# Kernel optimization log

Hardware: AMD Instinct MI355X
Metric: run time of the kernel (lower is better)

The kernel has to match this reference:

```python
import jax, jax.numpy as jnp
import numpy as np
from jax import lax

DN = ('NCHW', 'OIHW', 'NCHW')

def _conv(x, w, b):
    y = lax.conv_general_dilated(x, w, (1, 1), 'SAME', dimension_numbers=DN)
    return y + b[None, :, None, None]

def setup_inputs() -> dict:
    key = jax.random.key(0)
    ks = jax.random.split(key, 12)
    B, C, H, W = 8, 32, 128, 128
    Cb, INT, K, FK = 64, 64, 3, 3
    inp = {
        'z': jax.random.normal(ks[0], (B, C, H, W), jnp.float32),
        'backbone': jax.random.normal(ks[1], (B, Cb, H, W), jnp.float32),
        'mem_stab': jax.random.normal(ks[2], (B, C, H, W), jnp.float32),
        'mem_unstab': jax.random.normal(ks[3], (B, C, H, W), jnp.float32),
        'w0': jax.random.normal(ks[4], (INT, Cb + 3 * C, K, K), jnp.float32) * 0.05,
        'b0': jnp.zeros((INT,), jnp.float32),
        'w1': jax.random.normal(ks[5], (INT, INT, K, K), jnp.float32) * 0.05,
        'b1': jnp.zeros((INT,), jnp.float32),
        'w2': jax.random.normal(ks[6], (INT, INT, K, K), jnp.float32) * 0.05,
        'b2': jnp.zeros((INT,), jnp.float32),
        'w_last': jax.random.normal(ks[7], (C * FK * FK, INT, K, K), jnp.float32) * 0.05,
        'b_last': jnp.full((C * FK * FK,), -4.0, jnp.float32),
        'fusion_kernel_size': FK,
    }
    return inp

def reference(z, backbone, mem_stab, mem_unstab, w0, b0, w1, b1, w2, b2, w_last, b_last, fusion_kernel_size):
    B, C, H, W = z.shape
    k = int(fusion_kernel_size)
    p = k * k
    # controller conv stack (LeakyReLU slope 0.01, matching nn.LeakyReLU default)
    q = jnp.concatenate([backbone, z, mem_stab, mem_unstab], axis=1)
    q = jax.nn.leaky_relu(_conv(q, w0, b0), 0.01)
    q = jax.nn.leaky_relu(_conv(q, w1, b1), 0.01)
    q = jax.nn.leaky_relu(_conv(q, w2, b2), 0.01)
    # fusion head -> [B, C, p, HW]
    head = _conv(q, w_last, b_last).reshape(B, C, p, H * W)
    # softmax over p kernel positions + one extra logit-0 slot for z itself
    eta = jax.nn.softmax(jnp.concatenate([head, jnp.zeros_like(head[:, :, :1])], axis=2), axis=2)
    # unfold(mem_stab, k, padding=k//2): patches ordered (c, kh, kw) like torch unfold
    pad = k // 2
    mpad = jnp.pad(mem_stab, ((0, 0), (0, 0), (pad, pad), (pad, pad)))
    patches = jnp.stack([mpad[:, :, i:i + H, j:j + W] for i in range(k) for j in range(k)], axis=2)
    patches = patches.reshape(B, C, p, H * W)
    z_flat = z.reshape(B, C, H * W)
    z_stab = (patches * eta[:, :, :p]).sum(axis=2) + eta[:, :, p] * z_flat
    return z_stab.reshape(B, C, H, W)
```

## Files before the change

### kernel.cpp

```cpp
#include <hip/hip_runtime.h>
#include <hip/hip_fp16.h>

typedef _Float16 half8 __attribute__((ext_vector_type(8)));
typedef _Float16 half4v __attribute__((ext_vector_type(4)));
typedef float floatx4 __attribute__((ext_vector_type(4)));

#define HW 128
#define IMG (HW * HW)
#define PH 130
#define XP 164

typedef __attribute__((address_space(3))) _Float16 lds_f16;
typedef __attribute__((address_space(1))) const _Float16 glb_f16;
__device__ __forceinline__ void gload16(const _Float16* g, _Float16* l) {
    __builtin_amdgcn_global_load_lds((glb_f16*)g, (lds_f16*)l, 16, 0, 0);
}

__global__ void pack_w_all(const float* __restrict__ w0, const float* __restrict__ w1,
                           const float* __restrict__ w2, const float* __restrict__ wl,
                           _Float16* __restrict__ p0, _Float16* __restrict__ p1,
                           _Float16* __restrict__ p2, _Float16* __restrict__ pl) {
    int idx = blockIdx.x * 256 + threadIdx.x;
    if (idx < 92160) {
        int local = idx;
        int o = local / 1440;
        int rem = local % 1440;
        int c = rem / 9;
        int t = rem % 9;
        int oh = o >> 5, n = (o >> 4) & 1, l15 = o & 15;
        int cb = c >> 5, l4 = (c >> 3) & 3, e = c & 7;
        int frag = (t * 5 + cb) * 2 + n;
        p0[(size_t)oh * 46080 + frag * 512 + (l4 * 16 + l15) * 8 + e] =
            (_Float16)w0[local];
        return;
    }
    if (idx < 165888) {
        const float* w; _Float16* p; int local;
        if (idx < 129024) { w = w1; p = p1; local = idx - 92160; }
        else              { w = w2; p = p2; local = idx - 129024; }
        int o = local / 576;
        int rem = local % 576;
        int c = rem / 9;
        int t = rem % 9;
        int oh = o >> 5, n = (o >> 4) & 1, l15 = o & 15;
        int cb = c >> 5, l4 = (c >> 3) & 3, e = c & 7;
        int frag = t * 4 + cb * 2 + n;
        p[(size_t)oh * 18432 + frag * 512 + (l4 * 16 + l15) * 8 + e] =
            (_Float16)w[local];
        return;
    }
    if (idx < 331776) {
        int local = idx - 165888;
        int of = local / 576;
        int rem = local % 576;
        int c = rem / 9;
        int t = rem % 9;
        int ct = of / 96, o = of % 96;
        int og = o / 48;
        int n = (o % 48) / 16;
        int l15 = o & 15;
        int j = c >> 3;
        int cb = j >> 2, l4 = j & 3, e = c & 7;
        int frag = t * 2 + cb;
        pl[((((size_t)(ct * 2 + og) * 18 + frag) * 3 + n) * 64
            + (l4 * 16 + l15)) * 8 + e] = (_Float16)wl[local];
    }
}

__device__ __forceinline__ void zero_halo(_Float16* P, int C, int id) {
    int nvec = C / 8;
    int b = id / (516 * nvec);
    int r = id % (516 * nvec);
    int cell = r / nvec;
    int v = r % nvec;
    int hh, ww;
    if (cell < 130)      { hh = 0;   ww = cell; }
    else if (cell < 260) { hh = 129; ww = cell - 130; }
    else if (cell < 388) { hh = cell - 260 + 1; ww = 0; }
    else                 { hh = cell - 388 + 1; ww = 129; }
    half8 z8 = {};
    *reinterpret_cast<half8*>(P + (((size_t)b * PH + hh) * PH + ww) * C + v * 8) = z8;
}

__global__ void zero_pads_pre(_Float16* __restrict__ X0, _Float16* __restrict__ Q1) {
    int id = blockIdx.x * 256 + threadIdx.x;
    if (id < 82560) zero_halo(X0, 160, id);
    else if (id < 115584) zero_halo(Q1, 64, id - 82560);
}

__global__ void zero_pads64(_Float16* __restrict__ P) {
    int id = blockIdx.x * 256 + threadIdx.x;
    if (id < 33024) zero_halo(P, 64, id);
}

__global__ __launch_bounds__(256)
void pack_in(const float* __restrict__ z, const float* __restrict__ bb,
             const float* __restrict__ ms, const float* __restrict__ mu,
             _Float16* __restrict__ X0) {
    __shared__ _Float16 lds[160 * 132];
    int b = blockIdx.x >> 7;
    int h = blockIdx.x & 127;
    int tid = threadIdx.x;

    for (int i = 0; i < 20; i++) {
        int id = i * 256 + tid;
        int c = id >> 5;
        int col = (id & 31) * 4;
        const float* src; int cs; int csz;
        if (c < 64)       { src = bb; cs = c;       csz = 64; }
        else if (c < 96)  { src = z;  cs = c - 64;  csz = 32; }
        else if (c < 128) { src = ms; cs = c - 96;  csz = 32; }
        else              { src = mu; cs = c - 128; csz = 32; }
        float4 v = *reinterpret_cast<const float4*>(
            src + ((size_t)b * csz + cs) * IMG + h * HW + col);
        half4v hv = { (_Float16)v.x, (_Float16)v.y, (_Float16)v.z, (_Float16)v.w };
        *reinterpret_cast<half4v*>(&lds[c * 132 + col]) = hv;
    }
    __syncthreads();
    _Float16* dst = X0 + (((size_t)b * PH + (h + 1)) * PH + 1) * 160;
    for (int i = 0; i < 10; i++) {
        int id = i * 256 + tid;
        int pix = id / 20;
        int c0 = (id % 20) * 8;
        half8 hv;
        #pragma unroll
        for (int e = 0; e < 8; e++) hv[e] = lds[(c0 + e) * 132 + pix];
        *reinterpret_cast<half8*>(dst + (size_t)pix * 160 + c0) = hv;
    }
}

__global__ __launch_bounds__(256, 2)
void conv3_c160(const _Float16* __restrict__ X, const _Float16* __restrict__ Wp,
                const float* __restrict__ bias, _Float16* __restrict__ Y) {
    __shared__ _Float16 xs[130 * XP];
    int b = blockIdx.x >> 7;
    int h = blockIdx.x & 127;
    int tid = threadIdx.x;
    int lane = tid & 63;
    int wave = tid >> 6;
    int ph = wave & 1;
    int oh = wave >> 1;
    int l15 = lane & 15;
    int l4  = lane >> 4;

    floatx4 acc[4][2] = {};
    half8 SA[10], SB[10];

    const _Float16* wl = Wp + (size_t)oh * 46080 + lane * 8;

#define LOADW(S, k) { \
    _Pragma("unroll") \
    for (int cb = 0; cb < 5; cb++) \
      _Pragma("unroll") \
      for (int n = 0; n < 2; n++) \
        S[cb * 2 + n] = *reinterpret_cast<const half8*>( \
            wl + (size_t)(((k) * 5 + cb) * 2 + n) * 512); }

#define STAGE160(r) { \
    const _Float16* grow = X + ((size_t)b * PH + (h + (r))) * PH * 160; \
    _Pragma("unroll") \
    for (int i = 0; i < 11; i++) { \
      int id = i * 256 + tid; \
      if (id < 2600) { \
        half8 v = *reinterpret_cast<const half8*>(grow + (size_t)id * 8); \
        *reinterpret_cast<half8*>(&xs[(id / 20) * XP + (id % 20) * 8]) = v; \
      } } }

#define COMP160(dw, S) { \
    _Pragma("unroll") \
    for (int cb = 0; cb < 5; cb++) { \
      int kofs = cb * 32 + l4 * 8; \
      half8 af[4]; \
      _Pragma("unroll") \
      for (int m = 0; m < 4; m++) { \
        int p = ph * 64 + m * 16 + l15; \
        af[m] = *reinterpret_cast<const half8*>(&xs[(p + (dw)) * XP + kofs]); \
      } \
      _Pragma("unroll") \
      for (int m = 0; m < 4; m++) \
        _Pragma("unroll") \
        for (int n = 0; n < 2; n++) \
          acc[m][n] = __builtin_amdgcn_mfma_f32_16x16x32_f16( \
              af[m], S[cb * 2 + n], acc[m][n], 0, 0, 0); } }

    LOADW(SA, 0);
    STAGE160(0);
    __syncthreads();
    LOADW(SB, 1);  COMP160(0, SA);
    LOADW(SA, 2);  COMP160(1, SB);
    LOADW(SB, 3);  COMP160(2, SA);
    __syncthreads();
    STAGE160(1);
    __syncthreads();
    LOADW(SA, 4);  COMP160(0, SB);
    LOADW(SB, 5);  COMP160(1, SA);
    LOADW(SA, 6);  COMP160(2, SB);
    __syncthreads();
    STAGE160(2);
    __syncthreads();
    LOADW(SB, 7);  COMP160(0, SA);
    LOADW(SA, 8);  COMP160(1, SB);
    COMP160(2, SA);

#undef LOADW
#undef STAGE160
#undef COMP160

    _Float16* dst = Y + (((size_t)b * PH + (h + 1)) * PH + 1) * 64;
    #pragma unroll
    for (int m = 0; m < 4; m++)
        #pragma unroll
        for (int n = 0; n < 2; n++) {
            int o = oh * 32 + n * 16 + l15;
            float bv = bias[o];
            #pragma unroll
            for (int q = 0; q < 4; q++) {
                int pix = ph * 64 + m * 16 + l4 * 4 + q;
                float v = acc[m][n][q] + bv;
                v = v > 0.f ? v : 0.01f * v;
                dst[(size_t)pix * 64 + o] = (_Float16)v;
            }
        }
}

__global__ __launch_bounds__(256, 2)
void conv3_c64(const _Float16* __restrict__ X, const _Float16* __restrict__ Wp,
               const float* __restrict__ bias, _Float16* __restrict__ Y) {
    __shared__ _Float16 xs[130 * 72];
    int b = blockIdx.x >> 7;
    int h = blockIdx.x & 127;
    int tid = threadIdx.x;
    int lane = tid & 63;
    int wave = tid >> 6;
    int ph = wave & 1;
    int oh = wave >> 1;
    int l15 = lane & 15;
    int l4  = lane >> 4;

    floatx4 acc[4][2] = {};
    half8 SA[4], SB[4];

    const _Float16* wl = Wp + (size_t)oh * 18432 + lane * 8;
    const _Float16* xbase = X + ((size_t)b * PH + h) * (PH * 64);

#define LOADW1(S, k) { \
    _Pragma("unroll") \
    for (int cb = 0; cb < 2; cb++) \
      _Pragma("unroll") \
      for (int n = 0; n < 2; n++) \
        S[cb * 2 + n] = *reinterpret_cast<const half8*>( \
            wl + (size_t)((k) * 4 + cb * 2 + n) * 512); }

#define STAGE64(r) { \
    const _Float16* grow = xbase + (size_t)(r) * (PH * 64); \
    _Pragma("unroll") \
    for (int i = 0; i < 5; i++) { \
      int id = i * 256 + tid; \
      if (id < 1040) { \
        half8 v = *reinterpret_cast<const half8*>(grow + (size_t)id * 8); \
        *reinterpret_cast<half8*>(&xs[(id >> 3) * 72 + (id & 7) * 8]) = v; \
      } } }

#define COMP64(dw, S) { \
    _Pragma("unroll") \
    for (int cb = 0; cb < 2; cb++) { \
      int kofs = cb * 32 + l4 * 8; \
      half8 af[4]; \
      _Pragma("unroll") \
      for (int m = 0; m < 4; m++) { \
        int p = ph * 64 + m * 16 + l15; \
        af[m] = *reinterpret_cast<const half8*>(&xs[(p + (dw)) * 72 + kofs]); \
      } \
      _Pragma("unroll") \
      for (int m = 0; m < 4; m++) \
        _Pragma("unroll") \
        for (int n = 0; n < 2; n++) \
          acc[m][n] = __builtin_amdgcn_mfma_f32_16x16x32_f16( \
              af[m], S[cb * 2 + n], acc[m][n], 0, 0, 0); } }

    LOADW1(SA, 0);
    STAGE64(0);
    __syncthreads();
    LOADW1(SB, 1);  COMP64(0, SA);
    LOADW1(SA, 2);  COMP64(1, SB);
    LOADW1(SB, 3);  COMP64(2, SA);
    __syncthreads();
    STAGE64(1);
    __syncthreads();
    LOADW1(SA, 4);  COMP64(0, SB);
    LOADW1(SB, 5);  COMP64(1, SA);
    LOADW1(SA, 6);  COMP64(2, SB);
    __syncthreads();
    STAGE64(2);
    __syncthreads();
    LOADW1(SB, 7);  COMP64(0, SA);
    LOADW1(SA, 8);  COMP64(1, SB);
    COMP64(2, SA);

#undef LOADW1
#undef STAGE64
#undef COMP64

    _Float16* dst = Y + (((size_t)b * PH + (h + 1)) * PH + 1) * 64;
    #pragma unroll
    for (int m = 0; m < 4; m++)
        #pragma unroll
        for (int n = 0; n < 2; n++) {
            int o = oh * 32 + n * 16 + l15;
            float bv = bias[o];
            #pragma unroll
            for (int q = 0; q < 4; q++) {
                int pix = ph * 64 + m * 16 + l4 * 4 + q;
                float v = acc[m][n][q] + bv;
                v = v > 0.f ? v : 0.01f * v;
                dst[(size_t)pix * 64 + o] = (_Float16)v;
            }
        }
}

__global__ __launch_bounds__(256, 2)
void head_gemm(const _Float16* __restrict__ X, const _Float16* __restrict__ Wp,
               const float* __restrict__ b_last, _Float16* __restrict__ Lg,
               int bbase) {
    __shared__ _Float16 smem[12672];
    _Float16* xs = smem;
    _Float16* tb = smem;
    int blk = blockIdx.x;
    int ct = blk >> 9;
    int bi = (blk >> 7) & 3;
    int h  = blk & 127;
    int b = bbase + bi;
    int tid = threadIdx.x;
    int lane = tid & 63;
    int wave = tid >> 6;
    int pxh = wave & 1;
    int og  = wave >> 1;
    int l15 = lane & 15;
    int l4  = lane >> 4;

    floatx4 acc[4][3] = {};
    half8 SA[3], SB[3];

    const _Float16* wlh = Wp + ((size_t)ct * 2 + og) * 27648 + lane * 8;
    const _Float16* xbase = X + ((size_t)b * PH + h) * (PH * 64);

#define LOADWH(S, k, cb) { \
    _Pragma("unroll") \
    for (int n = 0; n < 3; n++) \
      S[n] = *reinterpret_cast<const half8*>( \
          wlh + (size_t)(((k) * 2 + (cb)) * 3 + n) * 512); }

#define STAGEH(r) { \
    const _Float16* xrow = xbase + (size_t)(r) * (PH * 64); \
    _Pragma("unroll") \
    for (int i = 0; i < 5; i++) { \
      int sbase = i * 256 + wave * 64; \
      int s = sbase + lane; \
      if (s < 1040) { \
        int px = s >> 3; \
        int j = (s & 7) ^ (px & 7); \
        gload16(xrow + (size_t)(px * 8 + j) * 8, xs + (size_t)sbase * 8); \
      } } }

#define COMPH(dw, cb, S) { \
    int j = (cb) * 4 + l4; \
    half8 af[4]; \
    _Pragma("unroll") \
    for (int m = 0; m < 4; m++) { \
      int px = pxh * 64 + m * 16 + l15 + (dw); \
      af[m] = *reinterpret_cast<const half8*>( \
          &xs[px * 64 + (j ^ (px & 7)) * 8]); \
    } \
    _Pragma("unroll") \
    for (int m = 0; m < 4; m++) \
      _Pragma("unroll") \
      for (int n = 0; n < 3; n++) \
        acc[m][n] = __builtin_amdgcn_mfma_f32_16x16x32_f16( \
            af[m], S[n], acc[m][n], 0, 0, 0); }

    LOADWH(SA, 0, 0);
    STAGEH(0);
    __syncthreads();
    LOADWH(SB, 0, 1);  COMPH(0, 0, SA);
    LOADWH(SA, 1, 0);  COMPH(0, 1, SB);
    LOADWH(SB, 1, 1);  COMPH(1, 0, SA);
    LOADWH(SA, 2, 0);  COMPH(1, 1, SB);
    LOADWH(SB, 2, 1);  COMPH(2, 0, SA);
    LOADWH(SA, 3, 0);  COMPH(2, 1, SB);
    __syncthreads();
    STAGEH(1);
    __syncthreads();
    LOADWH(SB, 3, 1);  COMPH(0, 0, SA);
    LOADWH(SA, 4, 0);  COMPH(0, 1, SB);
    LOADWH(SB, 4, 1);  COMPH(1, 0, SA);
    LOADWH(SA, 5, 0);  COMPH(1, 1, SB);
    LOADWH(SB, 5, 1);  COMPH(2, 0, SA);
    LOADWH(SA, 6, 0);  COMPH(2, 1, SB);
    __syncthreads();
    STAGEH(2);
    __syncthreads();
    LOADWH(SB, 6, 1);  COMPH(0, 0, SA);
    LOADWH(SA, 7, 0);  COMPH(0, 1, SB);
    LOADWH(SB, 7, 1);  COMPH(1, 0, SA);
    LOADWH(SA, 8, 0);  COMPH(1, 1, SB);
    LOADWH(SB, 8, 1);  COMPH(2, 0, SA);
    COMPH(2, 1, SB);

#undef LOADWH
#undef STAGEH
#undef COMPH

    __syncthreads();

    #pragma unroll
    for (int m = 0; m < 4; m++)
        #pragma unroll
        for (int n = 0; n < 3; n++) {
            int od = og * 48 + n * 16 + l15;
            float bv = b_last[ct * 96 + od];
            half4v hv;
            #pragma unroll
            for (int q = 0; q < 4; q++) hv[q] = (_Float16)(acc[m][n][q] + bv);
            *reinterpret_cast<half4v*>(&tb[od * 132 + pxh * 64 + m * 16 + l4 * 4]) = hv;
        }
    __syncthreads();

    _Float16* dst = Lg + (((size_t)bi * 128 + h) * 288 + (size_t)ct * 96) * 128;
    #pragma unroll
    for (int i = 0; i < 6; i++) {
        int id = i * 256 + tid;
        int od = id >> 4;
        int sl = id & 15;
        half8 v = *reinterpret_cast<const half8*>(&tb[od * 132 + sl * 8]);
        *reinterpret_cast<half8*>(dst + (size_t)od * 128 + sl * 8) = v;
    }
}

__global__ __launch_bounds__(256)
void fuse_sm(const _Float16* __restrict__ Lg, const float* __restrict__ ms,
             const float* __restrict__ zin, float* __restrict__ out, int bbase) {
    int blk = blockIdx.x;
    int bi = blk >> 11;
    int c  = (blk >> 6) & 31;
    int hp = blk & 63;
    int tid = threadIdx.x;
    int h = hp * 2 + (tid >> 7);
    int w = tid & 127;
    int b = bbase + bi;

    const _Float16* lrow = Lg + (((size_t)bi * 128 + h) * 288 + (size_t)c * 9) * 128 + w;
    float L[9];
    float mx = 0.f;
    #pragma unroll
    for (int j = 0; j < 9; j++) { L[j] = (float)lrow[j * 128]; mx = fmaxf(mx, L[j]); }
    float ez = __expf(-mx);
    float sum = ez;
    float e[9];
    #pragma unroll
    for (int j = 0; j < 9; j++) { e[j] = __expf(L[j] - mx); sum += e[j]; }
    float inv = 1.f / sum;
    const float* msb = ms + ((size_t)b * 32 + c) * IMG;
    float accv = ez * inv * zin[((size_t)b * 32 + c) * IMG + h * HW + w];
    #pragma unroll
    for (int kh = 0; kh < 3; kh++) {
        int h2 = h + kh - 1;
        int h2c = min(max(h2, 0), 127);
        bool okh = (unsigned)h2 < 128u;
        #pragma unroll
        for (int kw = 0; kw < 3; kw++) {
            int w2 = w + kw - 1;
            int w2c = min(max(w2, 0), 127);
            bool okw = (unsigned)w2 < 128u;
            float mv = msb[h2c * HW + w2c];
            accv += e[kh * 3 + kw] * inv * ((okh && okw) ? mv : 0.f);
        }
    }
    out[((size_t)b * 32 + c) * IMG + h * HW + w] = accv;
}

extern "C" void kernel_launch(void* const* d_in, const int* in_sizes, int n_in,
                              void* d_out, int out_size, void* d_ws, size_t ws_size,
                              hipStream_t stream) {
    const float* z  = (const float*)d_in[0];
    const float* bb = (const float*)d_in[1];
    const float* ms = (const float*)d_in[2];
    const float* mu = (const float*)d_in[3];
    const float* w0 = (const float*)d_in[4];
    const float* b0 = (const float*)d_in[5];
    const float* w1 = (const float*)d_in[6];
    const float* b1 = (const float*)d_in[7];
    const float* w2 = (const float*)d_in[8];
    const float* b2 = (const float*)d_in[9];
    const float* wl = (const float*)d_in[10];
    const float* bl = (const float*)d_in[11];

    char* ws = (char*)d_ws;
    _Float16* Wp0 = (_Float16*)(ws + 0);
    _Float16* Wp1 = (_Float16*)(ws + 184320);
    _Float16* Wp2 = (_Float16*)(ws + 258048);
    _Float16* WpL = (_Float16*)(ws + 331776);
    _Float16* BufA = (_Float16*)(ws + 663552);
    _Float16* BufB = (_Float16*)(ws + 43927552);

    _Float16* X0 = BufA;
    _Float16* Q1 = BufB;
    _Float16* Q2 = BufA;
    _Float16* Q3 = BufB;
    _Float16* Lg = BufA;

    pack_w_all<<<(331776 + 255) / 256, 256, 0, stream>>>(w0, w1, w2, wl, Wp0, Wp1, Wp2, WpL);
    zero_pads_pre<<<(115584 + 255) / 256, 256, 0, stream>>>(X0, Q1);
    pack_in<<<1024, 256, 0, stream>>>(z, bb, ms, mu, X0);

    conv3_c160<<<1024, 256, 0, stream>>>(X0, Wp0, b0, Q1);
    zero_pads64<<<(33024 + 255) / 256, 256, 0, stream>>>(Q2);
    conv3_c64<<<1024, 256, 0, stream>>>(Q1, Wp1, b1, Q2);
    conv3_c64<<<1024, 256, 0, stream>>>(Q2, Wp2, b2, Q3);

    head_gemm<<<1536, 256, 0, stream>>>(Q3, WpL, bl, Lg, 0);
    fuse_sm<<<8192, 256, 0, stream>>>(Lg, ms, z, (float*)d_out, 0);
    head_gemm<<<1536, 256, 0, stream>>>(Q3, WpL, bl, Lg, 4);
    fuse_sm<<<8192, 256, 0, stream>>>(Lg, ms, z, (float*)d_out, 4);
}
```

Measured before the change: 181.7 us.

## Compute two output rows per block in first conv to reuse staged input rows

The first 160-channel conv now uses 512-thread blocks that each produce two adjacent output rows, with two wave groups sharing each staged input row in LDS. This stages four input rows per block instead of three rows per output row, cutting global reads of the padded input by about a third. In exchange each wave group idles through one of the four stage phases, and there are more barriers. Grid size halves to 512 blocks, which lowers parallelism and may reduce occupancy given the register pressure of 512 threads.

Result: no change. 185.0 us (+1.8%).

```diff
diff --git a/kernel.cpp b/kernel.cpp
--- a/kernel.cpp
+++ b/kernel.cpp
@@ -129,17 +129,18 @@
     }
 }
 
-__global__ __launch_bounds__(256, 2)
+__global__ __launch_bounds__(512, 2)
 void conv3_c160(const _Float16* __restrict__ X, const _Float16* __restrict__ Wp,
                 const float* __restrict__ bias, _Float16* __restrict__ Y) {
     __shared__ _Float16 xs[130 * XP];
-    int b = blockIdx.x >> 7;
-    int h = blockIdx.x & 127;
+    int b = blockIdx.x >> 6;
+    int h0 = (blockIdx.x & 63) * 2;
     int tid = threadIdx.x;
     int lane = tid & 63;
     int wave = tid >> 6;
+    int rg = wave >> 2;
     int ph = wave & 1;
-    int oh = wave >> 1;
+    int oh = (wave >> 1) & 1;
     int l15 = lane & 15;
     int l4  = lane >> 4;
 
@@ -156,11 +157,11 @@
         S[cb * 2 + n] = *reinterpret_cast<const half8*>( \
             wl + (size_t)(((k) * 5 + cb) * 2 + n) * 512); }
 
-#define STAGE160(r) { \
-    const _Float16* grow = X + ((size_t)b * PH + (h + (r))) * PH * 160; \
-    _Pragma("unroll") \
-    for (int i = 0; i < 11; i++) { \
-      int id = i * 256 + tid; \
+#define STAGE160(g) { \
+    const _Float16* grow = X + ((size_t)b * PH + (h0 + (g))) * PH * 160; \
+    _Pragma("unroll") \
+    for (int i = 0; i < 6; i++) { \
+      int id = i * 512 + tid; \
       if (id < 2600) { \
         half8 v = *reinterpret_cast<const half8*>(grow + (size_t)id * 8); \
         *reinterpret_cast<half8*>(&xs[(id / 20) * XP + (id % 20) * 8]) = v; \
@@ -186,27 +187,51 @@
     LOADW(SA, 0);
     STAGE160(0);
     __syncthreads();
-    LOADW(SB, 1);  COMP160(0, SA);
-    LOADW(SA, 2);  COMP160(1, SB);
-    LOADW(SB, 3);  COMP160(2, SA);
+    if (rg == 0) {
+        LOADW(SB, 1);  COMP160(0, SA);
+        LOADW(SA, 2);  COMP160(1, SB);
+        LOADW(SB, 3);  COMP160(2, SA);
+    } else {
+        LOADW(SB, 1);
+    }
     __syncthreads();
     STAGE160(1);
     __syncthreads();
-    LOADW(SA, 4);  COMP160(0, SB);
-    LOADW(SB, 5);  COMP160(1, SA);
-    LOADW(SA, 6);  COMP160(2, SB);
+    if (rg == 0) {
+        LOADW(SA, 4);  COMP160(0, SB);
+        LOADW(SB, 5);  COMP160(1, SA);
+        LOADW(SA, 6);  COMP160(2, SB);
+    } else {
+        COMP160(0, SA);  LOADW(SA, 2);
+        COMP160(1, SB);  LOADW(SB, 3);
+        COMP160(2, SA);
+    }
     __syncthreads();
     STAGE160(2);
     __syncthreads();
-    LOADW(SB, 7);  COMP160(0, SA);
-    LOADW(SA, 8);  COMP160(1, SB);
-    COMP160(2, SA);
+    if (rg == 0) {
+        LOADW(SB, 7);  COMP160(0, SA);
+        LOADW(SA, 8);  COMP160(1, SB);
+        COMP160(2, SA);
+    } else {
+        LOADW(SA, 4);  COMP160(0, SB);
+        LOADW(SB, 5);  COMP160(1, SA);
+        LOADW(SA, 6);  COMP160(2, SB);
+    }
+    __syncthreads();
+    STAGE160(3);
+    __syncthreads();
+    if (rg == 1) {
+        LOADW(SB, 7);  COMP160(0, SA);
+        LOADW(SA, 8);  COMP160(1, SB);
+        COMP160(2, SA);
+    }
 
 #undef LOADW
 #undef STAGE160
 #undef COMP160
 
-    _Float16* dst = Y + (((size_t)b * PH + (h + 1)) * PH + 1) * 64;
+    _Float16* dst = Y + (((size_t)b * PH + (h0 + rg + 1)) * PH + 1) * 64;
     #pragma unroll
     for (int m = 0; m < 4; m++)
         #pragma unroll
@@ -512,7 +537,7 @@
     zero_pads_pre<<<(115584 + 255) / 256, 256, 0, stream>>>(X0, Q1);
     pack_in<<<1024, 256, 0, stream>>>(z, bb, ms, mu, X0);
 
-    conv3_c160<<<1024, 256, 0, stream>>>(X0, Wp0, b0, Q1);
+    conv3_c160<<<512, 512, 0, stream>>>(X0, Wp0, b0, Q1);
     zero_pads64<<<(33024 + 255) / 256, 256, 0, stream>>>(Q2);
     conv3_c64<<<1024, 256, 0, stream>>>(Q1, Wp1, b1, Q2);
     conv3_c64<<<1024, 256, 0, stream>>>(Q2, Wp2, b2, Q3);
```

## Fuse softmax-weighted unfold into head GEMM epilogue, handle straddling channels separately

Applied to the files above, without the earlier changes.

The head GEMM epilogue now computes the softmax and the 3x3 weighted sum directly from the logits tile in LDS for the channels fully contained in each 96-row output tile. It writes only the logits of the two channels that straddle tile boundaries (channels 10 and 21) to a small scratch buffer, and a small follow-up kernel finishes those. This removes most of the global round trip of the fp16 logits tensor and shrinks the separate fuse launch. The cost is a longer epilogue in the GEMM kernel, which may lower its occupancy or add latency.

Result: faster. 166.9 us (-8.2%).

```diff
diff --git a/kernel.cpp b/kernel.cpp
--- a/kernel.cpp
+++ b/kernel.cpp
@@ -319,9 +319,10 @@
 }
 
 __global__ __launch_bounds__(256, 2)
-void head_gemm(const _Float16* __restrict__ X, const _Float16* __restrict__ Wp,
-               const float* __restrict__ b_last, _Float16* __restrict__ Lg,
-               int bbase) {
+void head_fused(const _Float16* __restrict__ X, const _Float16* __restrict__ Wp,
+                const float* __restrict__ b_last, const float* __restrict__ ms,
+                const float* __restrict__ zin, float* __restrict__ out,
+                _Float16* __restrict__ Ls, int bbase) {
     __shared__ _Float16 smem[12672];
     _Float16* xs = smem;
     _Float16* tb = smem;
@@ -425,30 +426,73 @@
         }
     __syncthreads();
 
-    _Float16* dst = Lg + (((size_t)bi * 128 + h) * 288 + (size_t)ct * 96) * 128;
-    #pragma unroll
-    for (int i = 0; i < 6; i++) {
-        int id = i * 256 + tid;
-        int od = id >> 4;
-        int sl = id & 15;
-        half8 v = *reinterpret_cast<const half8*>(&tb[od * 132 + sl * 8]);
-        *reinterpret_cast<half8*>(dst + (size_t)od * 128 + sl * 8) = v;
+    if (tid < 96) {
+        int rowi = tid >> 4;
+        int sl = tid & 15;
+        int localrow, slot;
+        if (ct == 0)      { localrow = 90 + rowi; slot = rowi; }
+        else if (ct == 1) { localrow = (rowi < 3) ? rowi : 90 + rowi;
+                            slot = 6 + rowi; }
+        else              { localrow = rowi; slot = 12 + rowi; }
+        half8 v = *reinterpret_cast<const half8*>(&tb[localrow * 132 + sl * 8]);
+        *reinterpret_cast<half8*>(
+            Ls + (((size_t)(bi * 128 + h) * 18 + slot) * 128 + sl * 8)) = v;
+    }
+
+    #pragma unroll
+    for (int i = 0; i < 5; i++) {
+        int idx = i * 256 + tid;
+        int cidx = idx >> 7;
+        int px = idx & 127;
+        int c = (ct == 0) ? cidx : ((ct == 1) ? 11 + cidx : 22 + cidx);
+        int lbase = c * 9 - ct * 96;
+        float L[9];
+        float mx = 0.f;
+        #pragma unroll
+        for (int j = 0; j < 9; j++) {
+            L[j] = (float)tb[(lbase + j) * 132 + px];
+            mx = fmaxf(mx, L[j]);
+        }
+        float ez = __expf(-mx);
+        float sum = ez;
+        float e[9];
+        #pragma unroll
+        for (int j = 0; j < 9; j++) { e[j] = __expf(L[j] - mx); sum += e[j]; }
+        float inv = 1.f / sum;
+        const float* msb = ms + ((size_t)b * 32 + c) * IMG;
+        float accv = ez * inv * zin[((size_t)b * 32 + c) * IMG + h * HW + px];
+        #pragma unroll
+        for (int kh = 0; kh < 3; kh++) {
+            int h2 = h + kh - 1;
+            int h2c = min(max(h2, 0), 127);
+            bool okh = (unsigned)h2 < 128u;
+            #pragma unroll
+            for (int kw = 0; kw < 3; kw++) {
+                int w2 = px + kw - 1;
+                int w2c = min(max(w2, 0), 127);
+                bool okw = (unsigned)w2 < 128u;
+                float mv = msb[h2c * HW + w2c];
+                accv += e[kh * 3 + kw] * inv * ((okh && okw) ? mv : 0.f);
+            }
+        }
+        out[((size_t)b * 32 + c) * IMG + h * HW + px] = accv;
     }
 }
 
 __global__ __launch_bounds__(256)
-void fuse_sm(const _Float16* __restrict__ Lg, const float* __restrict__ ms,
-             const float* __restrict__ zin, float* __restrict__ out, int bbase) {
+void fuse_strad(const _Float16* __restrict__ Ls, const float* __restrict__ ms,
+                const float* __restrict__ zin, float* __restrict__ out, int bbase) {
     int blk = blockIdx.x;
-    int bi = blk >> 11;
-    int c  = (blk >> 6) & 31;
-    int hp = blk & 63;
+    int bi = blk >> 7;
+    int h = blk & 127;
     int tid = threadIdx.x;
-    int h = hp * 2 + (tid >> 7);
-    int w = tid & 127;
+    int cs = tid >> 7;
+    int px = tid & 127;
+    int c = cs ? 21 : 10;
+    int sb = cs ? 9 : 0;
     int b = bbase + bi;
 
-    const _Float16* lrow = Lg + (((size_t)bi * 128 + h) * 288 + (size_t)c * 9) * 128 + w;
+    const _Float16* lrow = Ls + (((size_t)(bi * 128 + h) * 18 + sb) * 128) + px;
     float L[9];
     float mx = 0.f;
     #pragma unroll
@@ -460,7 +504,7 @@
     for (int j = 0; j < 9; j++) { e[j] = __expf(L[j] - mx); sum += e[j]; }
     float inv = 1.f / sum;
     const float* msb = ms + ((size_t)b * 32 + c) * IMG;
-    float accv = ez * inv * zin[((size_t)b * 32 + c) * IMG + h * HW + w];
+    float accv = ez * inv * zin[((size_t)b * 32 + c) * IMG + h * HW + px];
     #pragma unroll
     for (int kh = 0; kh < 3; kh++) {
         int h2 = h + kh - 1;
@@ -468,14 +512,14 @@
         bool okh = (unsigned)h2 < 128u;
         #pragma unroll
         for (int kw = 0; kw < 3; kw++) {
-            int w2 = w + kw - 1;
+            int w2 = px + kw - 1;
             int w2c = min(max(w2, 0), 127);
             bool okw = (unsigned)w2 < 128u;
             float mv = msb[h2c * HW + w2c];
             accv += e[kh * 3 + kw] * inv * ((okh && okw) ? mv : 0.f);
         }
     }
-    out[((size_t)b * 32 + c) * IMG + h * HW + w] = accv;
+    out[((size_t)b * 32 + c) * IMG + h * HW + px] = accv;
 }
 
 extern "C" void kernel_launch(void* const* d_in, const int* in_sizes, int n_in,
@@ -506,7 +550,7 @@
     _Float16* Q1 = BufB;
     _Float16* Q2 = BufA;
     _Float16* Q3 = BufB;
-    _Float16* Lg = BufA;
+    _Float16* Ls = BufA;
 
     pack_w_all<<<(331776 + 255) / 256, 256, 0, stream>>>(w0, w1, w2, wl, Wp0, Wp1, Wp2, WpL);
     zero_pads_pre<<<(115584 + 255) / 256, 256, 0, stream>>>(X0, Q1);
@@ -517,8 +561,8 @@
     conv3_c64<<<1024, 256, 0, stream>>>(Q1, Wp1, b1, Q2);
     conv3_c64<<<1024, 256, 0, stream>>>(Q2, Wp2, b2, Q3);
 
-    head_gemm<<<1536, 256, 0, stream>>>(Q3, WpL, bl, Lg, 0);
-    fuse_sm<<<8192, 256, 0, stream>>>(Lg, ms, z, (float*)d_out, 0);
-    head_gemm<<<1536, 256, 0, stream>>>(Q3, WpL, bl, Lg, 4);
-    fuse_sm<<<8192, 256, 0, stream>>>(Lg, ms, z, (float*)d_out, 4);
-}
+    head_fused<<<1536, 256, 0, stream>>>(Q3, WpL, bl, ms, z, (float*)d_out, Ls, 0);
+    fuse_strad<<<512, 256, 0, stream>>>(Ls, ms, z, (float*)d_out, 0);
+    head_fused<<<1536, 256, 0, stream>>>(Q3, WpL, bl, ms, z, (float*)d_out, Ls, 4);
+    fuse_strad<<<512, 256, 0, stream>>>(Ls, ms, z, (float*)d_out, 4);
+}
```

## Fuse head GEMM with softmax-weighted fusion, keeping logits in LDS

Applied to the files above, without the earlier changes.

Merges the head convolution and the softmax/unfold fusion into one kernel. Each block now computes 144 output channels (16 full channel groups of 9 logits) with 6 waves, so softmax can run directly from LDS instead of writing fp16 logits to global memory and reading them back. The two batch-half launches collapse into a single launch over all 8 batches. This removes the logits round trip and several launches, at the cost of larger blocks, more LDS per block, and an epilogue that reads mem_stab with uncoalesced 3x3 neighbourhood loads inside the GEMM kernel.

New measurement: 187.2 us. 1.03x slower.

```diff
diff --git a/kernel.cpp b/kernel.cpp
--- a/kernel.cpp
+++ b/kernel.cpp
@@ -55,14 +55,13 @@
         int rem = local % 576;
         int c = rem / 9;
         int t = rem % 9;
-        int ct = of / 96, o = of % 96;
-        int og = o / 48;
-        int n = (o % 48) / 16;
-        int l15 = o & 15;
+        int g = of / 48;
+        int n = (of % 48) / 16;
+        int l15 = of & 15;
         int j = c >> 3;
         int cb = j >> 2, l4 = j & 3, e = c & 7;
         int frag = t * 2 + cb;
-        pl[((((size_t)(ct * 2 + og) * 18 + frag) * 3 + n) * 64
+        pl[((((size_t)g * 18 + frag) * 3 + n) * 64
             + (l4 * 16 + l15)) * 8 + e] = (_Float16)wl[local];
     }
 }
@@ -318,18 +317,17 @@
         }
 }
 
-__global__ __launch_bounds__(256, 2)
-void head_gemm(const _Float16* __restrict__ X, const _Float16* __restrict__ Wp,
-               const float* __restrict__ b_last, _Float16* __restrict__ Lg,
-               int bbase) {
-    __shared__ _Float16 smem[12672];
+__global__ __launch_bounds__(384, 2)
+void head_fused(const _Float16* __restrict__ X, const _Float16* __restrict__ Wp,
+                const float* __restrict__ b_last, const float* __restrict__ ms,
+                const float* __restrict__ zin, float* __restrict__ out) {
+    __shared__ _Float16 smem[19008];
     _Float16* xs = smem;
     _Float16* tb = smem;
     int blk = blockIdx.x;
-    int ct = blk >> 9;
-    int bi = (blk >> 7) & 3;
+    int ct = blk >> 10;
+    int b  = (blk >> 7) & 7;
     int h  = blk & 127;
-    int b = bbase + bi;
     int tid = threadIdx.x;
     int lane = tid & 63;
     int wave = tid >> 6;
@@ -341,7 +339,7 @@
     floatx4 acc[4][3] = {};
     half8 SA[3], SB[3];
 
-    const _Float16* wlh = Wp + ((size_t)ct * 2 + og) * 27648 + lane * 8;
+    const _Float16* wlh = Wp + ((size_t)ct * 3 + og) * 27648 + lane * 8;
     const _Float16* xbase = X + ((size_t)b * PH + h) * (PH * 64);
 
 #define LOADWH(S, k, cb) { \
@@ -353,8 +351,8 @@
 #define STAGEH(r) { \
     const _Float16* xrow = xbase + (size_t)(r) * (PH * 64); \
     _Pragma("unroll") \
-    for (int i = 0; i < 5; i++) { \
-      int sbase = i * 256 + wave * 64; \
+    for (int i = 0; i < 3; i++) { \
+      int sbase = i * 384 + wave * 64; \
       int s = sbase + lane; \
       if (s < 1040) { \
         int px = s >> 3; \
@@ -417,7 +415,7 @@
         #pragma unroll
         for (int n = 0; n < 3; n++) {
             int od = og * 48 + n * 16 + l15;
-            float bv = b_last[ct * 96 + od];
+            float bv = b_last[ct * 144 + od];
             half4v hv;
             #pragma unroll
             for (int q = 0; q < 4; q++) hv[q] = (_Float16)(acc[m][n][q] + bv);
@@ -425,57 +423,45 @@
         }
     __syncthreads();
 
-    _Float16* dst = Lg + (((size_t)bi * 128 + h) * 288 + (size_t)ct * 96) * 128;
-    #pragma unroll
     for (int i = 0; i < 6; i++) {
-        int id = i * 256 + tid;
-        int od = id >> 4;
-        int sl = id & 15;
-        half8 v = *reinterpret_cast<const half8*>(&tb[od * 132 + sl * 8]);
-        *reinterpret_cast<half8*>(dst + (size_t)od * 128 + sl * 8) = v;
-    }
-}
-
-__global__ __launch_bounds__(256)
-void fuse_sm(const _Float16* __restrict__ Lg, const float* __restrict__ ms,
-             const float* __restrict__ zin, float* __restrict__ out, int bbase) {
-    int blk = blockIdx.x;
-    int bi = blk >> 11;
-    int c  = (blk >> 6) & 31;
-    int hp = blk & 63;
-    int tid = threadIdx.x;
-    int h = hp * 2 + (tid >> 7);
-    int w = tid & 127;
-    int b = bbase + bi;
-
-    const _Float16* lrow = Lg + (((size_t)bi * 128 + h) * 288 + (size_t)c * 9) * 128 + w;
-    float L[9];
-    float mx = 0.f;
-    #pragma unroll
-    for (int j = 0; j < 9; j++) { L[j] = (float)lrow[j * 128]; mx = fmaxf(mx, L[j]); }
-    float ez = __expf(-mx);
-    float sum = ez;
-    float e[9];
-    #pragma unroll
-    for (int j = 0; j < 9; j++) { e[j] = __expf(L[j] - mx); sum += e[j]; }
-    float inv = 1.f / sum;
-    const float* msb = ms + ((size_t)b * 32 + c) * IMG;
-    float accv = ez * inv * zin[((size_t)b * 32 + c) * IMG + h * HW + w];
-    #pragma unroll
-    for (int kh = 0; kh < 3; kh++) {
-        int h2 = h + kh - 1;
-        int h2c = min(max(h2, 0), 127);
-        bool okh = (unsigned)h2 < 128u;
-        #pragma unroll
-        for (int kw = 0; kw < 3; kw++) {
-            int w2 = w + kw - 1;
-            int w2c = min(max(w2, 0), 127);
-            bool okw = (unsigned)w2 < 128u;
-            float mv = msb[h2c * HW + w2c];
-            accv += e[kh * 3 + kw] * inv * ((okh && okw) ? mv : 0.f);
+        int idx = i * 384 + tid;
+        if (idx < 2048) {
+            int cidx = idx >> 7;
+            int px = idx & 127;
+            int c = ct * 16 + cidx;
+            int lbase = cidx * 9;
+            float L[9];
+            float mx = 0.f;
+            #pragma unroll
+            for (int j = 0; j < 9; j++) {
+                L[j] = (float)tb[(lbase + j) * 132 + px];
+                mx = fmaxf(mx, L[j]);
+            }
+            float ez = __expf(-mx);
+            float sum = ez;
+            float e[9];
+            #pragma unroll
+            for (int j = 0; j < 9; j++) { e[j] = __expf(L[j] - mx); sum += e[j]; }
+            float inv = 1.f / sum;
+            const float* msb = ms + ((size_t)b * 32 + c) * IMG;
+            float accv = ez * inv * zin[((size_t)b * 32 + c) * IMG + h * HW + px];
+            #pragma unroll
+            for (int kh = 0; kh < 3; kh++) {
+                int h2 = h + kh - 1;
+                int h2c = min(max(h2, 0), 127);
+                bool okh = (unsigned)h2 < 128u;
+                #pragma unroll
+                for (int kw = 0; kw < 3; kw++) {
+                    int w2 = px + kw - 1;
+                    int w2c = min(max(w2, 0), 127);
+                    bool okw = (unsigned)w2 < 128u;
+                    float mv = msb[h2c * HW + w2c];
+                    accv += e[kh * 3 + kw] * inv * ((okh && okw) ? mv : 0.f);
+                }
+            }
+            out[((size_t)b * 32 + c) * IMG + h * HW + px] = accv;
         }
     }
-    out[((size_t)b * 32 + c) * IMG + h * HW + w] = accv;
 }
 
 extern "C" void kernel_launch(void* const* d_in, const int* in_sizes, int n_in,
@@ -506,7 +492,6 @@
     _Float16* Q1 = BufB;
     _Float16* Q2 = BufA;
     _Float16* Q3 = BufB;
-    _Float16* Lg = BufA;
 
     pack_w_all<<<(331776 + 255) / 256, 256, 0, stream>>>(w0, w1, w2, wl, Wp0, Wp1, Wp2, WpL);
     zero_pads_pre<<<(115584 + 255) / 256, 256, 0, stream>>>(X0, Q1);
@@ -517,8 +502,5 @@
     conv3_c64<<<1024, 256, 0, stream>>>(Q1, Wp1, b1, Q2);
     conv3_c64<<<1024, 256, 0, stream>>>(Q2, Wp2, b2, Q3);
 
-    head_gemm<<<1536, 256, 0, stream>>>(Q3, WpL, bl, Lg, 0);
-    fuse_sm<<<8192, 256, 0, stream>>>(Lg, ms, z, (float*)d_out, 0);
-    head_gemm<<<1536, 256, 0, stream>>>(Q3, WpL, bl, Lg, 4);
-    fuse_sm<<<8192, 256, 0, stream>>>(Lg, ms, z, (float*)d_out, 4);
-}
+    head_fused<<<2048, 384, 0, stream>>>(Q3, WpL, bl, ms, z, (float*)d_out);
+}
```
